# Performance work log

Measured on AMD Instinct MI355X. Metric: run time of the kernel, lower is better.

## Reference

```python
import jax, jax.numpy as jnp
import numpy as np

B, T, F, H, O = 64, 4096, 100, 200, 1


def setup_inputs() -> dict:
    key = jax.random.key(0)
    ks = jax.random.split(key, 7)
    s_i = 1.0 / np.sqrt(F)
    s_h = 1.0 / np.sqrt(H)
    return {
        "x": jax.random.normal(ks[0], (B, T, F), dtype=jnp.float32),
        # input-to-hidden weights for gates [r, z, n], concatenated: [F, 3H]
        "Wi": jax.random.uniform(ks[1], (F, 3 * H), jnp.float32, -s_i, s_i),
        "bi": jnp.zeros((3 * H,), jnp.float32),
        # hidden-to-hidden weights for gates [r, z, n]: [H, 3H] (no bias for r,z in flax GRUCell)
        "Wh": jax.random.uniform(ks[2], (H, 3 * H), jnp.float32, -s_h, s_h),
        "bhn": jnp.zeros((H,), jnp.float32),  # bias only on the h->n projection
        "Wo": jax.random.uniform(ks[3], (H, O), jnp.float32, -s_h, s_h),
        "bo": jnp.zeros((O,), jnp.float32),
    }


def _gru_forward(x, Wi, bi, Wh, bhn):
    # Precompute input projections for all timesteps: [B, T, 3H]
    gi_all = jnp.einsum("btf,fg->btg", x, Wi) + bi
    gi_all = jnp.transpose(gi_all, (1, 0, 2))  # [T, B, 3H]
    h0 = jnp.zeros((x.shape[0], Wh.shape[0]), x.dtype)

    def step(h, gi):
        hh = h @ Wh  # [B, 3H]
        r = jax.nn.sigmoid(gi[:, :H] + hh[:, :H])
        z = jax.nn.sigmoid(gi[:, H:2 * H] + hh[:, H:2 * H])
        n = jnp.tanh(gi[:, 2 * H:] + r * (hh[:, 2 * H:] + bhn))
        h_new = (1.0 - z) * n + z * h  # flax GRUCell convention
        return h_new, h_new

    _, hs = jax.lax.scan(step, h0, gi_all)  # hs: [T, B, H]
    return jnp.transpose(hs, (1, 0, 2))  # [B, T, H]


def reference(x, Wi, bi, Wh, bhn, Wo, bo):
    hs = _gru_forward(x, Wi, bi, Wh, bhn)
    return jnp.einsum("bth,ho->bto", hs, Wo) + bo  # [B, T, O]
```

## Files before the change

### kernel.cpp

```cpp
#include <hip/hip_runtime.h>
#include <cstdint>

#define B_  64
#define T_  4096
#define F_  100
#define H_  200
#define G_  600
#define KH_ 104

typedef _Float16 half2_t __attribute__((ext_vector_type(2)));

#define LDS_BARRIER() do {                                  \
    __builtin_amdgcn_sched_barrier(0);                      \
    asm volatile("s_waitcnt lgkmcnt(0)" ::: "memory");      \
    __builtin_amdgcn_s_barrier();                           \
    __builtin_amdgcn_sched_barrier(0);                      \
} while (0)

__device__ __forceinline__ float sigmoid_(float x) {
    return __builtin_amdgcn_rcpf(1.0f + __expf(-x));
}
__device__ __forceinline__ float tanh_(float x) {
    float e = __expf(-2.0f * x);
    return (1.0f - e) * __builtin_amdgcn_rcpf(1.0f + e);
}

__device__ __forceinline__ float fdot2_(half2_t a, half2_t b, float c) {
#if __has_builtin(__builtin_amdgcn_fdot2)
    return __builtin_amdgcn_fdot2(a, b, c, false);
#else
    return fmaf((float)a.x, (float)b.x, fmaf((float)a.y, (float)b.y, c));
#endif
}

__device__ __forceinline__ float dpp_xor1_add(float x) {
    int y = __builtin_amdgcn_update_dpp(0, __float_as_int(x), 0xB1, 0xF, 0xF, true);
    return x + __int_as_float(y);
}

__global__ void prep_whp(const float* __restrict__ Wh, half2_t* __restrict__ whp) {
    int i = blockIdx.x * 256 + threadIdx.x;
    if (i < KH_ * G_) {
        int k = i / G_, c = i - k * G_;
        half2_t v;
        v.x = (k < 100) ? (_Float16)Wh[(2 * k) * G_ + c] : (_Float16)0.f;
        v.y = (k < 100) ? (_Float16)Wh[(2 * k + 1) * G_ + c] : (_Float16)0.f;
        whp[i] = v;
    }
}

__global__ __launch_bounds__(640, 1)
void gi_kernel(const float* __restrict__ x, const float* __restrict__ Wi,
               const float* __restrict__ bi, float* __restrict__ gi,
               int t0, int TC) {
    __shared__ float xT[F_ * 68];
    int row0 = blockIdx.x * 64;
    int b    = row0 / TC;
    int tc0  = row0 - b * TC;
    const float* xrow = x + ((size_t)b * T_ + t0 + tc0) * F_;
    for (int i = threadIdx.x; i < 64 * F_; i += 640) {
        int r = i / F_, f = i - r * F_;
        xT[f * 68 + r] = xrow[i];
    }
    __syncthreads();
    int col = threadIdx.x < G_ ? threadIdx.x : G_ - 1;
    float acc[64];
    #pragma unroll
    for (int r = 0; r < 64; ++r) acc[r] = 0.f;
    for (int f = 0; f < F_; ++f) {
        float wi = Wi[f * G_ + col];
        const float4* xf = (const float4*)&xT[f * 68];
        #pragma unroll
        for (int q = 0; q < 16; ++q) {
            float4 v = xf[q];
            acc[4*q+0] = fmaf(v.x, wi, acc[4*q+0]);
            acc[4*q+1] = fmaf(v.y, wi, acc[4*q+1]);
            acc[4*q+2] = fmaf(v.z, wi, acc[4*q+2]);
            acc[4*q+3] = fmaf(v.w, wi, acc[4*q+3]);
        }
    }
    if (threadIdx.x < G_) {
        float bv = bi[col];
        float* grow = gi + (size_t)row0 * G_ + col;
        #pragma unroll 4
        for (int r = 0; r < 64; ++r) grow[(size_t)r * G_] = acc[r] + bv;
    }
}

__global__ __launch_bounds__(640, 1)
void scan_kernel(const float* __restrict__ gi, const half2_t* __restrict__ whp,
                 const float* __restrict__ bhn, _Float16* __restrict__ hs,
                 float* __restrict__ hstate, int TC, int first) {
    __shared__ __align__(16) _Float16 h_h[208];
    __shared__ float A_lds[G_];
    __shared__ float Hn_lds[H_];
    int b = blockIdx.x;
    int tid = threadIdx.x;
    int p = tid >> 1;
    int s = tid & 1;
    if (p >= 300) p = 299;
    int c0 = p;
    int c1 = p + 300;

    half2_t wa[52], wb[52];
    #pragma unroll
    for (int j = 0; j < 52; ++j) {
        wa[j] = whp[(52 * s + j) * G_ + c0];
        wb[j] = whp[(52 * s + j) * G_ + c1];
    }
    float bhn_r = (c1 >= 2*H_) ? bhn[c1 - 2*H_] : 0.f;

    float hj = 0.f;
    if (tid < H_) {
        hj = first ? 0.f : hstate[b * H_ + tid];
        h_h[tid] = (_Float16)hj;
    }
    if (tid >= H_ && tid < 208) h_h[tid] = (_Float16)0.f;
    __syncthreads();

    const float* girow = gi + (size_t)b * TC * G_;
    _Float16* hsb = hs + (size_t)b * TC * H_;

    float g0 = 0.f, g1 = 0.f;
    if (s == 0) { g0 = girow[c0]; g1 = girow[c1]; }
    for (int tc = 0; tc < TC; ++tc) {
        float g0n = 0.f, g1n = 0.f;
        if (s == 0 && tc + 1 < TC) {
            g0n = girow[(size_t)(tc + 1) * G_ + c0];
            g1n = girow[(size_t)(tc + 1) * G_ + c1];
        }
        float a0 = 0.f, a1 = 0.f, a2 = 0.f, a3 = 0.f;
        float b0 = 0.f, b1 = 0.f, b2 = 0.f, b3 = 0.f;
        const float4* h4 = (const float4*)(h_h + 104 * s);
        #pragma unroll
        for (int q = 0; q < 13; ++q) {
            float4 hv = h4[q];
            half2_t* hp = (half2_t*)&hv;
            a0 = fdot2_(hp[0], wa[4*q+0], a0);
            a1 = fdot2_(hp[1], wa[4*q+1], a1);
            a2 = fdot2_(hp[2], wa[4*q+2], a2);
            a3 = fdot2_(hp[3], wa[4*q+3], a3);
            b0 = fdot2_(hp[0], wb[4*q+0], b0);
            b1 = fdot2_(hp[1], wb[4*q+1], b1);
            b2 = fdot2_(hp[2], wb[4*q+2], b2);
            b3 = fdot2_(hp[3], wb[4*q+3], b3);
        }
        float accA = dpp_xor1_add((a0 + a1) + (a2 + a3));
        float accB = dpp_xor1_add((b0 + b1) + (b2 + b3));
        if (s == 0) {
            A_lds[c0] = g0 + accA;
            if (c1 < 2*H_) {
                A_lds[c1] = g1 + accB;
            } else {
                A_lds[c1] = g1;
                Hn_lds[c1 - 2*H_] = accB + bhn_r;
            }
        }
        LDS_BARRIER();
        if (tid < H_) {
            float r = sigmoid_(A_lds[tid]);
            float z = sigmoid_(A_lds[H_ + tid]);
            float n = tanh_(A_lds[2*H_ + tid] + r * Hn_lds[tid]);
            hj = n + z * (hj - n);
            h_h[tid] = (_Float16)hj;
            hsb[(size_t)tc * H_ + tid] = (_Float16)hj;
        }
        LDS_BARRIER();
        g0 = g0n; g1 = g1n;
    }
    if (tid < H_) hstate[b * H_ + tid] = hj;
}

__global__ __launch_bounds__(256, 4)
void outproj_kernel(const _Float16* __restrict__ hs, const float* __restrict__ Wo,
                    const float* __restrict__ bo, float* __restrict__ out,
                    int t0, int TC) {
    int r = blockIdx.x * 256 + threadIdx.x;
    if (r >= B_ * TC) return;
    int b = r / TC, tc = r - b * TC;
    const float4* h4 = (const float4*)(hs + (size_t)r * H_);
    float acc = 0.f;
    #pragma unroll
    for (int q = 0; q < 25; ++q) {
        float4 v = h4[q];
        const _Float16* hp = (const _Float16*)&v;
        #pragma unroll
        for (int j = 0; j < 8; ++j)
            acc = fmaf((float)hp[j], Wo[q * 8 + j], acc);
    }
    out[(size_t)b * T_ + t0 + tc] = acc + bo[0];
}

extern "C" void kernel_launch(void* const* d_in, const int* in_sizes, int n_in,
                              void* d_out, int out_size, void* d_ws, size_t ws_size,
                              hipStream_t stream) {
    const float* x   = (const float*)d_in[0];
    const float* Wi  = (const float*)d_in[1];
    const float* bi  = (const float*)d_in[2];
    const float* Wh  = (const float*)d_in[3];
    const float* bhn = (const float*)d_in[4];
    const float* Wo  = (const float*)d_in[5];
    const float* bo  = (const float*)d_in[6];
    float* out = (float*)d_out;

    const size_t hstate_b = (size_t)B_ * H_ * sizeof(float);
    const size_t whp_b    = (size_t)KH_ * G_ * sizeof(half2_t);
    int TC = T_;
    while (TC > 64 &&
           (size_t)B_ * TC * (G_ * 4 + H_ * 2) + hstate_b + whp_b > ws_size)
        TC >>= 1;
    char* p = (char*)d_ws;
    float*    gi     = (float*)p;            p += (size_t)B_ * TC * G_ * sizeof(float);
    _Float16* hsbuf  = (_Float16*)p;         p += (size_t)B_ * TC * H_ * sizeof(_Float16);
    float*    hstate = (float*)p;            p += hstate_b;
    half2_t*  whp    = (half2_t*)p;

    prep_whp<<<dim3((KH_ * G_ + 255) / 256), dim3(256), 0, stream>>>(Wh, whp);

    int nchunks = T_ / TC;
    for (int c = 0; c < nchunks; ++c) {
        int t0 = c * TC;
        gi_kernel<<<dim3(B_ * TC / 64), dim3(640), 0, stream>>>(x, Wi, bi, gi, t0, TC);
        scan_kernel<<<dim3(B_), dim3(640), 0, stream>>>(gi, whp, bhn, hsbuf,
                                                        hstate, TC, c == 0);
        outproj_kernel<<<dim3((B_ * TC + 255) / 256), dim3(256), 0, stream>>>(
            hsbuf, Wo, bo, out, t0, TC);
    }
}
```

Measured before the change: 5.403 ms.

## Remap GRU scan work to 4-lane quads computing five gate columns each

The recurrent scan kernel now splits each group of five gate columns across a quad of four lanes, each holding 28 packed half2 weight pairs per column in registers. Partial dot products are reduced with two DPP steps, and the block shrinks from 640 to 512 threads, padding K to 224. The goal is more reuse of each h vector load across several columns and fewer waves per barrier, at the cost of heavier register pressure (140 weight registers per thread) and some idle lanes.

Result: no change. 5.398 ms (-0.1%).

```diff
diff --git a/kernel.cpp b/kernel.cpp
--- a/kernel.cpp
+++ b/kernel.cpp
@@ -6,7 +6,8 @@
 #define F_  100
 #define H_  200
 #define G_  600
-#define KH_ 104
+#define KP_ 224
+#define KH_ 112
 
 typedef _Float16 half2_t __attribute__((ext_vector_type(2)));
 
@@ -33,9 +34,11 @@
 #endif
 }
 
-__device__ __forceinline__ float dpp_xor1_add(float x) {
-    int y = __builtin_amdgcn_update_dpp(0, __float_as_int(x), 0xB1, 0xF, 0xF, true);
-    return x + __int_as_float(y);
+__device__ __forceinline__ float quad_sum_(float x) {
+    int y1 = __builtin_amdgcn_update_dpp(0, __float_as_int(x), 0xB1, 0xF, 0xF, true);
+    x += __int_as_float(y1);
+    int y2 = __builtin_amdgcn_update_dpp(0, __float_as_int(x), 0x4E, 0xF, 0xF, true);
+    return x + __int_as_float(y2);
 }
 
 __global__ void prep_whp(const float* __restrict__ Wh, half2_t* __restrict__ whp) {
@@ -87,73 +90,89 @@
     }
 }
 
-__global__ __launch_bounds__(640, 1)
+__global__ __launch_bounds__(512, 1) __attribute__((amdgpu_waves_per_eu(2, 2)))
 void scan_kernel(const float* __restrict__ gi, const half2_t* __restrict__ whp,
                  const float* __restrict__ bhn, _Float16* __restrict__ hs,
                  float* __restrict__ hstate, int TC, int first) {
-    __shared__ __align__(16) _Float16 h_h[208];
+    __shared__ __align__(16) _Float16 h_h[KP_];
     __shared__ float A_lds[G_];
     __shared__ float Hn_lds[H_];
     int b = blockIdx.x;
     int tid = threadIdx.x;
-    int p = tid >> 1;
-    int s = tid & 1;
-    if (p >= 300) p = 299;
-    int c0 = p;
-    int c1 = p + 300;
-
-    half2_t wa[52], wb[52];
-    #pragma unroll
-    for (int j = 0; j < 52; ++j) {
-        wa[j] = whp[(52 * s + j) * G_ + c0];
-        wb[j] = whp[(52 * s + j) * G_ + c1];
-    }
-    float bhn_r = (c1 >= 2*H_) ? bhn[c1 - 2*H_] : 0.f;
+    int q = tid >> 2;
+    int l = tid & 3;
+    int qc = q < 120 ? q : 119;
+    bool act = q < 120;
+    int c0 = 5 * qc;
+
+    half2_t w[5][28];
+    {
+        const half2_t* wbase = whp + (size_t)(28 * l) * G_ + c0;
+        #pragma unroll
+        for (int k = 0; k < 28; ++k) {
+            #pragma unroll
+            for (int j = 0; j < 5; ++j)
+                w[j][k] = wbase[(size_t)k * G_ + j];
+        }
+    }
+    int ca = c0 + l;
+    int cb = c0 + 4;
+    float bhn_a = (ca >= 2*H_) ? bhn[ca - 2*H_] : 0.f;
+    float bhn_b = (l == 0 && cb >= 2*H_) ? bhn[cb - 2*H_] : 0.f;
 
     float hj = 0.f;
     if (tid < H_) {
         hj = first ? 0.f : hstate[b * H_ + tid];
         h_h[tid] = (_Float16)hj;
     }
-    if (tid >= H_ && tid < 208) h_h[tid] = (_Float16)0.f;
+    if (tid >= H_ && tid < KP_) h_h[tid] = (_Float16)0.f;
     __syncthreads();
 
     const float* girow = gi + (size_t)b * TC * G_;
     _Float16* hsb = hs + (size_t)b * TC * H_;
 
-    float g0 = 0.f, g1 = 0.f;
-    if (s == 0) { g0 = girow[c0]; g1 = girow[c1]; }
+    float ga = girow[ca];
+    float gb = (l == 0) ? girow[cb] : 0.f;
     for (int tc = 0; tc < TC; ++tc) {
-        float g0n = 0.f, g1n = 0.f;
-        if (s == 0 && tc + 1 < TC) {
-            g0n = girow[(size_t)(tc + 1) * G_ + c0];
-            g1n = girow[(size_t)(tc + 1) * G_ + c1];
-        }
-        float a0 = 0.f, a1 = 0.f, a2 = 0.f, a3 = 0.f;
-        float b0 = 0.f, b1 = 0.f, b2 = 0.f, b3 = 0.f;
-        const float4* h4 = (const float4*)(h_h + 104 * s);
-        #pragma unroll
-        for (int q = 0; q < 13; ++q) {
-            float4 hv = h4[q];
+        float gan = 0.f, gbn = 0.f;
+        if (tc + 1 < TC) {
+            const float* gnx = girow + (size_t)(tc + 1) * G_;
+            gan = gnx[ca];
+            if (l == 0) gbn = gnx[cb];
+        }
+        float pd0[5], pd1[5];
+        #pragma unroll
+        for (int j = 0; j < 5; ++j) { pd0[j] = 0.f; pd1[j] = 0.f; }
+        const float4* h4 = (const float4*)(h_h + 56 * l);
+        #pragma unroll
+        for (int k4 = 0; k4 < 7; ++k4) {
+            float4 hv = h4[k4];
             half2_t* hp = (half2_t*)&hv;
-            a0 = fdot2_(hp[0], wa[4*q+0], a0);
-            a1 = fdot2_(hp[1], wa[4*q+1], a1);
-            a2 = fdot2_(hp[2], wa[4*q+2], a2);
-            a3 = fdot2_(hp[3], wa[4*q+3], a3);
-            b0 = fdot2_(hp[0], wb[4*q+0], b0);
-            b1 = fdot2_(hp[1], wb[4*q+1], b1);
-            b2 = fdot2_(hp[2], wb[4*q+2], b2);
-            b3 = fdot2_(hp[3], wb[4*q+3], b3);
-        }
-        float accA = dpp_xor1_add((a0 + a1) + (a2 + a3));
-        float accB = dpp_xor1_add((b0 + b1) + (b2 + b3));
-        if (s == 0) {
-            A_lds[c0] = g0 + accA;
-            if (c1 < 2*H_) {
-                A_lds[c1] = g1 + accB;
+            #pragma unroll
+            for (int j = 0; j < 5; ++j) {
+                pd0[j] = fdot2_(hp[0], w[j][4*k4+0], pd0[j]);
+                pd1[j] = fdot2_(hp[1], w[j][4*k4+1], pd1[j]);
+                pd0[j] = fdot2_(hp[2], w[j][4*k4+2], pd0[j]);
+                pd1[j] = fdot2_(hp[3], w[j][4*k4+3], pd1[j]);
+            }
+        }
+        float tot[5];
+        #pragma unroll
+        for (int j = 0; j < 5; ++j) tot[j] = quad_sum_(pd0[j] + pd1[j]);
+        if (act) {
+            if (ca < 2*H_) {
+                A_lds[ca] = ga + tot[l];
             } else {
-                A_lds[c1] = g1;
-                Hn_lds[c1 - 2*H_] = accB + bhn_r;
+                A_lds[ca] = ga;
+                Hn_lds[ca - 2*H_] = tot[l] + bhn_a;
+            }
+            if (l == 0) {
+                if (cb < 2*H_) {
+                    A_lds[cb] = gb + tot[4];
+                } else {
+                    A_lds[cb] = gb;
+                    Hn_lds[cb - 2*H_] = tot[4] + bhn_b;
+                }
             }
         }
         LDS_BARRIER();
@@ -166,7 +185,7 @@
             hsb[(size_t)tc * H_ + tid] = (_Float16)hj;
         }
         LDS_BARRIER();
-        g0 = g0n; g1 = g1n;
+        ga = gan; gb = gbn;
     }
     if (tid < H_) hstate[b * H_ + tid] = hj;
 }
@@ -221,7 +240,7 @@
     for (int c = 0; c < nchunks; ++c) {
         int t0 = c * TC;
         gi_kernel<<<dim3(B_ * TC / 64), dim3(640), 0, stream>>>(x, Wi, bi, gi, t0, TC);
-        scan_kernel<<<dim3(B_), dim3(640), 0, stream>>>(gi, whp, bhn, hsbuf,
+        scan_kernel<<<dim3(B_), dim3(512), 0, stream>>>(gi, whp, bhn, hsbuf,
                                                         hstate, TC, c == 0);
         outproj_kernel<<<dim3((B_ * TC + 255) / 256), dim3(256), 0, stream>>>(
             hsbuf, Wo, bo, out, t0, TC);
```

## Fuse scan, next-chunk input projection and prior-chunk outproj into one pipelined kernel

Applied to the files above, without the earlier changes.

The time axis is split into chunks of 512, with double-buffered gi and hs buffers. A fused kernel assigns 64 blocks to the recurrent scan of chunk c, a second group of blocks to the input projection of chunk c+1, and a third to the output projection of chunk c-1. The aim is to hide the parallel projection work behind the latency-bound serial scan and to keep each chunk's working set small enough to stay cache-resident. The price is more kernel launches, a chunk-boundary state handoff, and a large padded shared-memory allocation so each block gets its own CU.

After: 4.665 ms, median of 2. 1.16x faster.

```diff
diff --git a/kernel.cpp b/kernel.cpp
--- a/kernel.cpp
+++ b/kernel.cpp
@@ -7,6 +7,7 @@
 #define H_  200
 #define G_  600
 #define KH_ 104
+#define SMEM_PAD 86016
 
 typedef _Float16 half2_t __attribute__((ext_vector_type(2)));
 
@@ -49,21 +50,22 @@
     }
 }
 
-__global__ __launch_bounds__(640, 1)
-void gi_kernel(const float* __restrict__ x, const float* __restrict__ Wi,
-               const float* __restrict__ bi, float* __restrict__ gi,
-               int t0, int TC) {
-    __shared__ float xT[F_ * 68];
-    int row0 = blockIdx.x * 64;
+__device__ __forceinline__
+void gi_body(char* smem, const float* __restrict__ x, const float* __restrict__ Wi,
+             const float* __restrict__ bi, float* __restrict__ gi,
+             int t0, int TC, int blk) {
+    float* xT = (float*)smem;
+    int tid = threadIdx.x;
+    int row0 = blk * 64;
     int b    = row0 / TC;
     int tc0  = row0 - b * TC;
     const float* xrow = x + ((size_t)b * T_ + t0 + tc0) * F_;
-    for (int i = threadIdx.x; i < 64 * F_; i += 640) {
+    for (int i = tid; i < 64 * F_; i += 640) {
         int r = i / F_, f = i - r * F_;
         xT[f * 68 + r] = xrow[i];
     }
     __syncthreads();
-    int col = threadIdx.x < G_ ? threadIdx.x : G_ - 1;
+    int col = tid < G_ ? tid : G_ - 1;
     float acc[64];
     #pragma unroll
     for (int r = 0; r < 64; ++r) acc[r] = 0.f;
@@ -79,7 +81,7 @@
             acc[4*q+3] = fmaf(v.w, wi, acc[4*q+3]);
         }
     }
-    if (threadIdx.x < G_) {
+    if (tid < G_) {
         float bv = bi[col];
         float* grow = gi + (size_t)row0 * G_ + col;
         #pragma unroll 4
@@ -87,14 +89,13 @@
     }
 }
 
-__global__ __launch_bounds__(640, 1)
-void scan_kernel(const float* __restrict__ gi, const half2_t* __restrict__ whp,
-                 const float* __restrict__ bhn, _Float16* __restrict__ hs,
-                 float* __restrict__ hstate, int TC, int first) {
-    __shared__ __align__(16) _Float16 h_h[208];
-    __shared__ float A_lds[G_];
-    __shared__ float Hn_lds[H_];
-    int b = blockIdx.x;
+__device__ __forceinline__
+void scan_body(char* smem, const float* __restrict__ gi, const half2_t* __restrict__ whp,
+               const float* __restrict__ bhn, _Float16* __restrict__ hs,
+               float* __restrict__ hstate, int TC, int first, int b) {
+    _Float16* h_h  = (_Float16*)smem;
+    float*    A_lds = (float*)(smem + 448);
+    float*    Hn_lds = (float*)(smem + 2848);
     int tid = threadIdx.x;
     int p = tid >> 1;
     int s = tid & 1;
@@ -171,6 +172,58 @@
     if (tid < H_) hstate[b * H_ + tid] = hj;
 }
 
+__device__ __forceinline__
+void out_body(const _Float16* __restrict__ hs, const float* __restrict__ Wo,
+              const float* __restrict__ bo, float* __restrict__ out,
+              int t0, int TC, int blk) {
+    int r = blk * 640 + threadIdx.x;
+    if (r >= B_ * TC) return;
+    int b = r / TC, tc = r - b * TC;
+    const float4* h4 = (const float4*)(hs + (size_t)r * H_);
+    float acc = 0.f;
+    #pragma unroll
+    for (int q = 0; q < 25; ++q) {
+        float4 v = h4[q];
+        const _Float16* hp = (const _Float16*)&v;
+        #pragma unroll
+        for (int j = 0; j < 8; ++j)
+            acc = fmaf((float)hp[j], Wo[q * 8 + j], acc);
+    }
+    out[(size_t)b * T_ + t0 + tc] = acc + bo[0];
+}
+
+__global__ __launch_bounds__(640, 1)
+void fused_kernel(const float* __restrict__ x, const float* __restrict__ Wi,
+                  const float* __restrict__ bi,
+                  const float* __restrict__ gi_scan, float* __restrict__ gi_next,
+                  const half2_t* __restrict__ whp, const float* __restrict__ bhn,
+                  _Float16* __restrict__ hs_w, const _Float16* __restrict__ hs_r,
+                  float* __restrict__ hstate,
+                  const float* __restrict__ Wo, const float* __restrict__ bo,
+                  float* __restrict__ out,
+                  int c, int nc, int TC) {
+    __shared__ __align__(16) char smem[SMEM_PAD];
+    int blk = blockIdx.x;
+    int gi_blocks = (B_ * TC) / 64;
+    if (blk < 64) {
+        scan_body(smem, gi_scan, whp, bhn, hs_w, hstate, TC, c == 0, blk);
+    } else if (blk < 64 + gi_blocks) {
+        if (c + 1 < nc)
+            gi_body(smem, x, Wi, bi, gi_next, (c + 1) * TC, TC, blk - 64);
+    } else {
+        if (c >= 1)
+            out_body(hs_r, Wo, bo, out, (c - 1) * TC, TC, blk - 64 - gi_blocks);
+    }
+}
+
+__global__ __launch_bounds__(640, 1)
+void gi_kernel(const float* __restrict__ x, const float* __restrict__ Wi,
+               const float* __restrict__ bi, float* __restrict__ gi,
+               int t0, int TC) {
+    __shared__ __align__(16) char smem[F_ * 68 * 4];
+    gi_body(smem, x, Wi, bi, gi, t0, TC, blockIdx.x);
+}
+
 __global__ __launch_bounds__(256, 4)
 void outproj_kernel(const _Float16* __restrict__ hs, const float* __restrict__ Wo,
                     const float* __restrict__ bo, float* __restrict__ out,
@@ -205,25 +258,39 @@
 
     const size_t hstate_b = (size_t)B_ * H_ * sizeof(float);
     const size_t whp_b    = (size_t)KH_ * G_ * sizeof(half2_t);
-    int TC = T_;
+    int TC = 512;
     while (TC > 64 &&
-           (size_t)B_ * TC * (G_ * 4 + H_ * 2) + hstate_b + whp_b > ws_size)
+           2 * (size_t)B_ * TC * (G_ * 4 + H_ * 2) + hstate_b + whp_b > ws_size)
         TC >>= 1;
+    int nc = T_ / TC;
     char* p = (char*)d_ws;
-    float*    gi     = (float*)p;            p += (size_t)B_ * TC * G_ * sizeof(float);
-    _Float16* hsbuf  = (_Float16*)p;         p += (size_t)B_ * TC * H_ * sizeof(_Float16);
+    const size_t gi_b = (size_t)B_ * TC * G_ * sizeof(float);
+    const size_t hs_b = (size_t)B_ * TC * H_ * sizeof(_Float16);
+    float*    gi0    = (float*)p;            p += gi_b;
+    float*    gi1    = (float*)p;            p += gi_b;
+    _Float16* hs0    = (_Float16*)p;         p += hs_b;
+    _Float16* hs1    = (_Float16*)p;         p += hs_b;
     float*    hstate = (float*)p;            p += hstate_b;
     half2_t*  whp    = (half2_t*)p;
 
     prep_whp<<<dim3((KH_ * G_ + 255) / 256), dim3(256), 0, stream>>>(Wh, whp);
 
-    int nchunks = T_ / TC;
-    for (int c = 0; c < nchunks; ++c) {
-        int t0 = c * TC;
-        gi_kernel<<<dim3(B_ * TC / 64), dim3(640), 0, stream>>>(x, Wi, bi, gi, t0, TC);
-        scan_kernel<<<dim3(B_), dim3(640), 0, stream>>>(gi, whp, bhn, hsbuf,
-                                                        hstate, TC, c == 0);
-        outproj_kernel<<<dim3((B_ * TC + 255) / 256), dim3(256), 0, stream>>>(
-            hsbuf, Wo, bo, out, t0, TC);
-    }
-}
+    int gi_blocks  = (B_ * TC) / 64;
+    int out_blocks = (B_ * TC + 639) / 640;
+    int grid = 64 + gi_blocks + out_blocks;
+
+    gi_kernel<<<dim3(gi_blocks), dim3(640), 0, stream>>>(x, Wi, bi, gi0, 0, TC);
+
+    for (int c = 0; c < nc; ++c) {
+        float*    gi_s = (c & 1) ? gi1 : gi0;
+        float*    gi_w = (c & 1) ? gi0 : gi1;
+        _Float16* hs_w = (c & 1) ? hs1 : hs0;
+        _Float16* hs_r = (c & 1) ? hs0 : hs1;
+        fused_kernel<<<dim3(grid), dim3(640), 0, stream>>>(
+            x, Wi, bi, gi_s, gi_w, whp, bhn, hs_w, hs_r, hstate,
+            Wo, bo, out, c, nc, TC);
+    }
+    _Float16* hs_last = ((nc - 1) & 1) ? hs1 : hs0;
+    outproj_kernel<<<dim3((B_ * TC + 255) / 256), dim3(256), 0, stream>>>(
+        hs_last, Wo, bo, out, (nc - 1) * TC, TC);
+}
```
